# Optimization experiments

Measured on AMD Instinct MI355X. Metric: run time of the kernel, lower is better.

The kernel has to match this reference:

```python
import jax, jax.numpy as jnp
import numpy as np

IN_DIM = 128
KEY_F = 64
VAL_F = 128  # must equal IN_DIM for the residual
B, L = 8, 2048


def setup_inputs() -> dict:
    key = jax.random.key(0)
    ks = jax.random.split(key, 7)
    s_in = 1.0 / np.sqrt(IN_DIM)
    x = jax.random.normal(ks[0], (B, IN_DIM, L), dtype=jnp.float32)
    # Conv1d kernel_size=1 weights stored as [out, in]
    Wq = jax.random.uniform(ks[1], (KEY_F, IN_DIM), jnp.float32, -s_in, s_in)
    bq = jax.random.uniform(ks[2], (KEY_F,), jnp.float32, -s_in, s_in)
    Wk = jax.random.uniform(ks[3], (KEY_F, IN_DIM), jnp.float32, -s_in, s_in)
    bk = jax.random.uniform(ks[4], (KEY_F,), jnp.float32, -s_in, s_in)
    Wv = jax.random.uniform(ks[5], (VAL_F, IN_DIM), jnp.float32, -s_in, s_in)
    bv = jax.random.uniform(ks[6], (VAL_F,), jnp.float32, -s_in, s_in)
    gamma = jnp.zeros((1,), dtype=jnp.float32)
    return {"x": x, "Wq": Wq, "bq": bq, "Wk": Wk, "bk": bk, "Wv": Wv, "bv": bv, "gamma": gamma}


def reference(x, Wq, bq, Wk, bk, Wv, bv, gamma):
    # 1x1 conv projections: [B, C, L] -> [B, F, L]
    q = jnp.einsum('fc,bcl->bfl', Wq, x) + bq[None, :, None]
    k = jnp.einsum('fc,bcl->bfl', Wk, x) + bk[None, :, None]
    v = jnp.einsum('fc,bcl->bfl', Wv, x) + bv[None, :, None]
    # energy[b, i, j] = sum_f q[b, f, i] * k[b, f, j]  -> [B, L, L]
    energy = jnp.einsum('bfi,bfj->bij', q, k)
    attn = jax.nn.softmax(energy, axis=-1)
    # out[b, f, i] = sum_j attn[b, i, j] * v[b, f, j]
    out = jnp.einsum('bij,bfj->bfi', attn, v)
    return gamma * out + x
```

## Files before the change

### kernel.cpp

```cpp
#include <hip/hip_runtime.h>
#include <hip/hip_bf16.h>

#define LL 2048
#define NB 8
#define L2E 1.4426950408889634f

typedef float f32x4 __attribute__((ext_vector_type(4)));
typedef short s16x8 __attribute__((ext_vector_type(8)));
typedef unsigned int u32;

__device__ __forceinline__ unsigned short f2bf(float f) {
  u32 u = __float_as_uint(f);
  return (unsigned short)((u + 0x7FFFu + ((u >> 16) & 1u)) >> 16);
}

__global__ __launch_bounds__(256, 1) void proj_kernel(
    const float* __restrict__ x,
    const float* __restrict__ Wq, const float* __restrict__ bq,
    const float* __restrict__ Wk, const float* __restrict__ bk,
    const float* __restrict__ Wv, const float* __restrict__ bv,
    unsigned short* __restrict__ Qt,
    unsigned short* __restrict__ Kt,
    unsigned short* __restrict__ Vf)
{
  __shared__ float4 Wl[256 * 32];
  __shared__ float  bl[256];

  const int t = threadIdx.x;
  const float4* wq4 = (const float4*)Wq;
  const float4* wk4 = (const float4*)Wk;
  const float4* wv4 = (const float4*)Wv;
  #pragma unroll
  for (int i = 0; i < 8; ++i)  Wl[i * 256 + t]        = wq4[i * 256 + t];
  #pragma unroll
  for (int i = 0; i < 8; ++i)  Wl[2048 + i * 256 + t] = wk4[i * 256 + t];
  #pragma unroll
  for (int i = 0; i < 16; ++i) Wl[4096 + i * 256 + t] = wv4[i * 256 + t];
  bl[t] = (t < 64) ? bq[t] : (t < 128) ? bk[t - 64] : bv[t - 128];
  __syncthreads();

  const int fg = t >> 6;
  const int l  = t & 63;
  const int b  = blockIdx.y;
  const int gl = blockIdx.x * 64 + l;

  float acc[64];
  #pragma unroll
  for (int i = 0; i < 64; ++i) acc[i] = 0.f;

  const float* xb = x + (size_t)b * 128 * LL + gl;

  for (int c0 = 0; c0 < 128; c0 += 4) {
    float x0 = xb[(c0 + 0) * LL];
    float x1 = xb[(c0 + 1) * LL];
    float x2 = xb[(c0 + 2) * LL];
    float x3 = xb[(c0 + 3) * LL];
    #pragma unroll
    for (int ff = 0; ff < 64; ++ff) {
      float4 wv4v = Wl[(fg * 64 + ff) * 32 + (c0 >> 2)];
      acc[ff] = fmaf(x0, wv4v.x, acc[ff]);
      acc[ff] = fmaf(x1, wv4v.y, acc[ff]);
      acc[ff] = fmaf(x2, wv4v.z, acc[ff]);
      acc[ff] = fmaf(x3, wv4v.w, acc[ff]);
    }
  }
  #pragma unroll
  for (int ff = 0; ff < 64; ++ff) acc[ff] += bl[fg * 64 + ff];

  if (fg < 2) {
    unsigned short* dst = (fg == 0 ? Qt : Kt) + ((size_t)b * LL + gl) * 64;
    #pragma unroll
    for (int v = 0; v < 8; ++v) {
      s16x8 pk;
      #pragma unroll
      for (int e = 0; e < 8; ++e) pk[e] = (short)f2bf(acc[v * 8 + e]);
      *(s16x8*)(dst + v * 8) = pk;
    }
  } else {
    unsigned short* dst = Vf + ((size_t)b * 128 + (size_t)(fg - 2) * 64) * LL + gl;
    #pragma unroll
    for (int ff = 0; ff < 64; ++ff) dst[(size_t)ff * LL] = f2bf(acc[ff]);
  }
}

__global__ __launch_bounds__(256, 1) void attn_kernel(
    const unsigned short* __restrict__ Qt,
    const unsigned short* __restrict__ Kt,
    const unsigned short* __restrict__ Vf,
    const float* __restrict__ x,
    const float* __restrict__ gammap,
    float* __restrict__ out)
{
  __shared__ uint4 ldsK4[64 * 8];
  __shared__ uint4 ldsV4[128 * 8];
  __shared__ __align__(16) unsigned short Plds[4][16][80];
  __shared__ float Olds[4][16][129];

  const int t    = threadIdx.x;
  const int w    = t >> 6;
  const int lane = t & 63;
  const int cn   = lane & 15;
  const int g    = lane >> 4;
  const int bid  = blockIdx.x;
  const int virt = (bid & 7) * 32 + (bid >> 3);
  const int b    = virt >> 5;
  const int i0   = (virt & 31) * 64;

  s16x8 qf[2];
  {
    const unsigned short* qp = Qt + ((size_t)b * LL + i0 + w * 16 + cn) * 64 + g * 8;
    qf[0] = *(const s16x8*)(qp);
    qf[1] = *(const s16x8*)(qp + 32);
  }

  const f32x4 zero4 = {0.f, 0.f, 0.f, 0.f};
  f32x4 accO[8];
  #pragma unroll
  for (int i = 0; i < 8; ++i) accO[i] = zero4;
  float mrow[4], lrow[4];
  #pragma unroll
  for (int r = 0; r < 4; ++r) { mrow[r] = -1e30f; lrow[r] = 0.f; }

  for (int jt = 0; jt < 32; ++jt) {
    const int j0 = jt * 64;
    __syncthreads();

    #pragma unroll
    for (int e = 0; e < 2; ++e) {
      int q = e * 256 + t, r = q >> 3, c = q & 7;
      uint4 d = *(const uint4*)(Kt + ((size_t)b * LL + j0 + r) * 64 + c * 8);
      ldsK4[r * 8 + (c ^ (r & 7))] = d;
    }
    #pragma unroll
    for (int e = 0; e < 4; ++e) {
      int q = e * 256 + t, r = q >> 3, c = q & 7;
      uint4 d = *(const uint4*)(Vf + ((size_t)b * 128 + r) * LL + j0 + c * 8);
      ldsV4[r * 8 + (c ^ (r & 7))] = d;
    }
    __syncthreads();

    f32x4 s[4];
    #pragma unroll
    for (int jb = 0; jb < 4; ++jb) s[jb] = zero4;
    #pragma unroll
    for (int kt = 0; kt < 2; ++kt) {
      #pragma unroll
      for (int jb = 0; jb < 4; ++jb) {
        int r = jb * 16 + cn;
        s16x8 kf = *(const s16x8*)&ldsK4[r * 8 + ((kt * 4 + g) ^ (cn & 7))];
        s[jb] = __builtin_amdgcn_mfma_f32_16x16x32_bf16(qf[kt], kf, s[jb], 0, 0, 0);
      }
    }

    float tm[4];
    #pragma unroll
    for (int r = 0; r < 4; ++r) {
      tm[r] = fmaxf(fmaxf(s[0][r], s[1][r]), fmaxf(s[2][r], s[3][r]));
      tm[r] = fmaxf(tm[r], __shfl_xor(tm[r], 1));
      tm[r] = fmaxf(tm[r], __shfl_xor(tm[r], 2));
      tm[r] = fmaxf(tm[r], __shfl_xor(tm[r], 4));
      tm[r] = fmaxf(tm[r], __shfl_xor(tm[r], 8));
    }
    float alpha[4];
    #pragma unroll
    for (int r = 0; r < 4; ++r) {
      float mn = fmaxf(mrow[r], tm[r]);
      alpha[r] = __builtin_amdgcn_exp2f((mrow[r] - mn) * L2E);
      mrow[r] = mn;
    }
    float rs[4] = {0.f, 0.f, 0.f, 0.f};
    float p[4][4];
    #pragma unroll
    for (int jb = 0; jb < 4; ++jb) {
      #pragma unroll
      for (int r = 0; r < 4; ++r) {
        float pv = __builtin_amdgcn_exp2f((s[jb][r] - mrow[r]) * L2E);
        p[jb][r] = pv;
        rs[r] += pv;
      }
    }
    #pragma unroll
    for (int r = 0; r < 4; ++r) {
      rs[r] += __shfl_xor(rs[r], 1);
      rs[r] += __shfl_xor(rs[r], 2);
      rs[r] += __shfl_xor(rs[r], 4);
      rs[r] += __shfl_xor(rs[r], 8);
      lrow[r] = lrow[r] * alpha[r] + rs[r];
    }
    #pragma unroll
    for (int fb = 0; fb < 8; ++fb) {
      #pragma unroll
      for (int r = 0; r < 4; ++r) accO[fb][r] *= alpha[r];
    }

    #pragma unroll
    for (int jb = 0; jb < 4; ++jb) {
      #pragma unroll
      for (int r = 0; r < 4; ++r)
        Plds[w][g * 4 + r][jb * 16 + cn] = f2bf(p[jb][r]);
    }

    #pragma unroll
    for (int kt = 0; kt < 2; ++kt) {
      s16x8 pa = *(const s16x8*)((const unsigned short*)&Plds[w][cn][0] + kt * 32 + g * 8);
      #pragma unroll
      for (int fb = 0; fb < 8; ++fb) {
        int f = fb * 16 + cn;
        s16x8 vf = *(const s16x8*)&ldsV4[f * 8 + ((kt * 4 + g) ^ (cn & 7))];
        accO[fb] = __builtin_amdgcn_mfma_f32_16x16x32_bf16(pa, vf, accO[fb], 0, 0, 0);
      }
    }
  }

  #pragma unroll
  for (int r = 0; r < 4; ++r) {
    float inv = 1.f / lrow[r];
    #pragma unroll
    for (int fb = 0; fb < 8; ++fb)
      Olds[w][g * 4 + r][fb * 16 + cn] = accO[fb][r] * inv;
  }
  __syncthreads();
  const float gamma = gammap[0];
  {
    const int r = cn;
    const int row = i0 + w * 16 + r;
    #pragma unroll
    for (int ff = 0; ff < 32; ++ff) {
      int f = ff * 4 + g;
      float val = Olds[w][r][f];
      size_t idx = ((size_t)b * 128 + f) * LL + row;
      out[idx] = gamma * val + x[idx];
    }
  }
}

extern "C" void kernel_launch(void* const* d_in, const int* in_sizes, int n_in,
                              void* d_out, int out_size, void* d_ws, size_t ws_size,
                              hipStream_t stream) {
  const float* x     = (const float*)d_in[0];
  const float* Wq    = (const float*)d_in[1];
  const float* bq    = (const float*)d_in[2];
  const float* Wk    = (const float*)d_in[3];
  const float* bk    = (const float*)d_in[4];
  const float* Wv    = (const float*)d_in[5];
  const float* bv    = (const float*)d_in[6];
  const float* gamma = (const float*)d_in[7];
  float* out = (float*)d_out;

  unsigned short* Qt = (unsigned short*)d_ws;
  unsigned short* Kt = Qt + (size_t)NB * LL * 64;
  unsigned short* Vf = Kt + (size_t)NB * LL * 64;

  proj_kernel<<<dim3(32, 8), 256, 0, stream>>>(x, Wq, bq, Wk, bk, Wv, bv, Qt, Kt, Vf);
  attn_kernel<<<dim3(256), 256, 0, stream>>>(Qt, Kt, Vf, x, gamma, out);
}
```

Before: 197.2 us.

## Use MFMA for projections and double-buffer K/V tiles in attention

The projection kernel is rewritten to use bf16 MFMA instructions. Weights go into register fragments and x is staged transposed into LDS as bf16, replacing the scalar fp32 FMA loop. The attention kernel now double-buffers its K/V LDS tiles: each tile's global loads are issued into registers before the current tile's compute and written to the other buffer afterwards, which removes one barrier per iteration and hides load latency. In exchange it uses more LDS and registers, and the projections are now computed in bf16 rather than fp32, which lowers their precision.

```diff
diff --git a/kernel.cpp b/kernel.cpp
--- a/kernel.cpp
+++ b/kernel.cpp
@@ -8,10 +8,15 @@
 typedef float f32x4 __attribute__((ext_vector_type(4)));
 typedef short s16x8 __attribute__((ext_vector_type(8)));
 typedef unsigned int u32;
+typedef unsigned int u32x2 __attribute__((ext_vector_type(2)));
+typedef unsigned int u32x4 __attribute__((ext_vector_type(4)));
 
 __device__ __forceinline__ unsigned short f2bf(float f) {
   u32 u = __float_as_uint(f);
   return (unsigned short)((u + 0x7FFFu + ((u >> 16) & 1u)) >> 16);
+}
+__device__ __forceinline__ u32 pack2(float a, float b) {
+  return (u32)f2bf(a) | ((u32)f2bf(b) << 16);
 }
 
 __global__ __launch_bounds__(256, 1) void proj_kernel(
@@ -23,63 +28,108 @@
     unsigned short* __restrict__ Kt,
     unsigned short* __restrict__ Vf)
 {
-  __shared__ float4 Wl[256 * 32];
-  __shared__ float  bl[256];
-
-  const int t = threadIdx.x;
-  const float4* wq4 = (const float4*)Wq;
-  const float4* wk4 = (const float4*)Wk;
-  const float4* wv4 = (const float4*)Wv;
-  #pragma unroll
-  for (int i = 0; i < 8; ++i)  Wl[i * 256 + t]        = wq4[i * 256 + t];
-  #pragma unroll
-  for (int i = 0; i < 8; ++i)  Wl[2048 + i * 256 + t] = wk4[i * 256 + t];
-  #pragma unroll
-  for (int i = 0; i < 16; ++i) Wl[4096 + i * 256 + t] = wv4[i * 256 + t];
+  __shared__ __align__(16) unsigned short xT[64 * 128];
+  __shared__ float bl[256];
+
+  const int t  = threadIdx.x;
+  const int w  = t >> 6;
+  const int ll = t & 63;
+  const int lane = t & 63;
+  const int cn = lane & 15;
+  const int g  = lane >> 4;
+  const int b  = blockIdx.x >> 5;
+  const int l0 = (blockIdx.x & 31) * 64;
+
+  const int f0 = w * 64;
+  s16x8 afr[4][4];
+  #pragma unroll
+  for (int fb = 0; fb < 4; ++fb) {
+    const int f = f0 + fb * 16 + cn;
+    const float* p = (f < 64) ? (Wq + (size_t)f * 128)
+                   : (f < 128) ? (Wk + (size_t)(f - 64) * 128)
+                               : (Wv + (size_t)(f - 128) * 128);
+    #pragma unroll
+    for (int kt = 0; kt < 4; ++kt) {
+      const float4 u = *(const float4*)(p + kt * 32 + g * 8);
+      const float4 v = *(const float4*)(p + kt * 32 + g * 8 + 4);
+      u32x4 pk = {pack2(u.x, u.y), pack2(u.z, u.w), pack2(v.x, v.y), pack2(v.z, v.w)};
+      afr[fb][kt] = __builtin_bit_cast(s16x8, pk);
+    }
+  }
+
+  {
+    const float* xb = x + (size_t)b * 128 * LL + l0 + ll;
+    #pragma unroll
+    for (int it = 0; it < 4; ++it) {
+      const int ch = it * 4 + w;
+      const float* p = xb + (size_t)ch * 8 * LL;
+      float v[8];
+      #pragma unroll
+      for (int j = 0; j < 8; ++j) v[j] = p[(size_t)j * LL];
+      u32x4 pk = {pack2(v[0], v[1]), pack2(v[2], v[3]),
+                  pack2(v[4], v[5]), pack2(v[6], v[7])};
+      *(u32x4*)&xT[ll * 128 + ((ch ^ (ll & 15)) * 8)] = pk;
+    }
+  }
   bl[t] = (t < 64) ? bq[t] : (t < 128) ? bk[t - 64] : bv[t - 128];
   __syncthreads();
 
-  const int fg = t >> 6;
-  const int l  = t & 63;
-  const int b  = blockIdx.y;
-  const int gl = blockIdx.x * 64 + l;
-
-  float acc[64];
-  #pragma unroll
-  for (int i = 0; i < 64; ++i) acc[i] = 0.f;
-
-  const float* xb = x + (size_t)b * 128 * LL + gl;
-
-  for (int c0 = 0; c0 < 128; c0 += 4) {
-    float x0 = xb[(c0 + 0) * LL];
-    float x1 = xb[(c0 + 1) * LL];
-    float x2 = xb[(c0 + 2) * LL];
-    float x3 = xb[(c0 + 3) * LL];
-    #pragma unroll
-    for (int ff = 0; ff < 64; ++ff) {
-      float4 wv4v = Wl[(fg * 64 + ff) * 32 + (c0 >> 2)];
-      acc[ff] = fmaf(x0, wv4v.x, acc[ff]);
-      acc[ff] = fmaf(x1, wv4v.y, acc[ff]);
-      acc[ff] = fmaf(x2, wv4v.z, acc[ff]);
-      acc[ff] = fmaf(x3, wv4v.w, acc[ff]);
-    }
-  }
-  #pragma unroll
-  for (int ff = 0; ff < 64; ++ff) acc[ff] += bl[fg * 64 + ff];
-
-  if (fg < 2) {
-    unsigned short* dst = (fg == 0 ? Qt : Kt) + ((size_t)b * LL + gl) * 64;
-    #pragma unroll
-    for (int v = 0; v < 8; ++v) {
-      s16x8 pk;
-      #pragma unroll
-      for (int e = 0; e < 8; ++e) pk[e] = (short)f2bf(acc[v * 8 + e]);
-      *(s16x8*)(dst + v * 8) = pk;
+  const f32x4 zero4 = {0.f, 0.f, 0.f, 0.f};
+  f32x4 acc[4][4];
+  #pragma unroll
+  for (int fb = 0; fb < 4; ++fb)
+    #pragma unroll
+    for (int lb = 0; lb < 4; ++lb) acc[fb][lb] = zero4;
+
+  #pragma unroll
+  for (int kt = 0; kt < 4; ++kt) {
+    s16x8 bfr[4];
+    #pragma unroll
+    for (int lb = 0; lb < 4; ++lb)
+      bfr[lb] = *(const s16x8*)&xT[(lb * 16 + cn) * 128 + (((kt * 4 + g) ^ cn) * 8)];
+    #pragma unroll
+    for (int fb = 0; fb < 4; ++fb)
+      #pragma unroll
+      for (int lb = 0; lb < 4; ++lb)
+        acc[fb][lb] = __builtin_amdgcn_mfma_f32_16x16x32_bf16(afr[fb][kt], bfr[lb], acc[fb][lb], 0, 0, 0);
+  }
+
+  #pragma unroll
+  for (int fb = 0; fb < 4; ++fb) {
+    float bb0 = bl[f0 + fb * 16 + 4 * g + 0];
+    float bb1 = bl[f0 + fb * 16 + 4 * g + 1];
+    float bb2 = bl[f0 + fb * 16 + 4 * g + 2];
+    float bb3 = bl[f0 + fb * 16 + 4 * g + 3];
+    #pragma unroll
+    for (int lb = 0; lb < 4; ++lb) {
+      acc[fb][lb][0] += bb0; acc[fb][lb][1] += bb1;
+      acc[fb][lb][2] += bb2; acc[fb][lb][3] += bb3;
+    }
+  }
+
+  if (w < 2) {
+    unsigned short* base = (w == 0 ? Qt : Kt) + (size_t)b * LL * 64;
+    #pragma unroll
+    for (int lb = 0; lb < 4; ++lb) {
+      const int l = l0 + lb * 16 + cn;
+      #pragma unroll
+      for (int fb = 0; fb < 4; ++fb) {
+        u32x2 pk = {pack2(acc[fb][lb][0], acc[fb][lb][1]),
+                    pack2(acc[fb][lb][2], acc[fb][lb][3])};
+        *(u32x2*)(base + (size_t)l * 64 + fb * 16 + 4 * g) = pk;
+      }
     }
   } else {
-    unsigned short* dst = Vf + ((size_t)b * 128 + (size_t)(fg - 2) * 64) * LL + gl;
-    #pragma unroll
-    for (int ff = 0; ff < 64; ++ff) dst[(size_t)ff * LL] = f2bf(acc[ff]);
+    unsigned short* base = Vf + ((size_t)b * 128 + (size_t)(w - 2) * 64) * LL;
+    #pragma unroll
+    for (int fb = 0; fb < 4; ++fb)
+      #pragma unroll
+      for (int lb = 0; lb < 4; ++lb) {
+        const int l = l0 + lb * 16 + cn;
+        #pragma unroll
+        for (int r = 0; r < 4; ++r)
+          base[(size_t)(fb * 16 + 4 * g + r) * LL + l] = f2bf(acc[fb][lb][r]);
+      }
   }
 }
 
@@ -91,9 +141,9 @@
     const float* __restrict__ gammap,
     float* __restrict__ out)
 {
-  __shared__ uint4 ldsK4[64 * 8];
-  __shared__ uint4 ldsV4[128 * 8];
-  __shared__ __align__(16) unsigned short Plds[4][16][80];
+  __shared__ uint4 ldsK4[2][64 * 8];
+  __shared__ uint4 ldsV4[2][128 * 8];
+  __shared__ __align__(16) unsigned short Plds[4][16][72];
   __shared__ float Olds[4][16][129];
 
   const int t    = threadIdx.x;
@@ -113,6 +163,28 @@
     qf[1] = *(const s16x8*)(qp + 32);
   }
 
+  uint4 kreg[2], vreg[4];
+  const int sr_k[2] = { t >> 3, (256 + t) >> 3 };
+  const int sc     = t & 7;
+  const int sr_v[4] = { t >> 3, (256 + t) >> 3, (512 + t) >> 3, (768 + t) >> 3 };
+
+  auto issue_loads = [&](int j0) {
+    #pragma unroll
+    for (int e = 0; e < 2; ++e)
+      kreg[e] = *(const uint4*)(Kt + ((size_t)b * LL + j0 + sr_k[e]) * 64 + sc * 8);
+    #pragma unroll
+    for (int e = 0; e < 4; ++e)
+      vreg[e] = *(const uint4*)(Vf + ((size_t)b * 128 + sr_v[e]) * LL + j0 + sc * 8);
+  };
+  auto write_lds = [&](uint4* K4, uint4* V4) {
+    #pragma unroll
+    for (int e = 0; e < 2; ++e)
+      K4[sr_k[e] * 8 + (sc ^ (sr_k[e] & 7))] = kreg[e];
+    #pragma unroll
+    for (int e = 0; e < 4; ++e)
+      V4[sr_v[e] * 8 + (sc ^ (sr_v[e] & 7))] = vreg[e];
+  };
+
   const f32x4 zero4 = {0.f, 0.f, 0.f, 0.f};
   f32x4 accO[8];
   #pragma unroll
@@ -121,23 +193,17 @@
   #pragma unroll
   for (int r = 0; r < 4; ++r) { mrow[r] = -1e30f; lrow[r] = 0.f; }
 
+  issue_loads(0);
+  write_lds(ldsK4[0], ldsV4[0]);
+
   for (int jt = 0; jt < 32; ++jt) {
-    const int j0 = jt * 64;
+    const int cur = jt & 1;
     __syncthreads();
 
-    #pragma unroll
-    for (int e = 0; e < 2; ++e) {
-      int q = e * 256 + t, r = q >> 3, c = q & 7;
-      uint4 d = *(const uint4*)(Kt + ((size_t)b * LL + j0 + r) * 64 + c * 8);
-      ldsK4[r * 8 + (c ^ (r & 7))] = d;
-    }
-    #pragma unroll
-    for (int e = 0; e < 4; ++e) {
-      int q = e * 256 + t, r = q >> 3, c = q & 7;
-      uint4 d = *(const uint4*)(Vf + ((size_t)b * 128 + r) * LL + j0 + c * 8);
-      ldsV4[r * 8 + (c ^ (r & 7))] = d;
-    }
-    __syncthreads();
+    if (jt + 1 < 32) issue_loads((jt + 1) * 64);
+
+    const uint4* K4 = ldsK4[cur];
+    const uint4* V4 = ldsV4[cur];
 
     f32x4 s[4];
     #pragma unroll
@@ -147,7 +213,7 @@
       #pragma unroll
       for (int jb = 0; jb < 4; ++jb) {
         int r = jb * 16 + cn;
-        s16x8 kf = *(const s16x8*)&ldsK4[r * 8 + ((kt * 4 + g) ^ (cn & 7))];
+        s16x8 kf = *(const s16x8*)&K4[r * 8 + ((kt * 4 + g) ^ (r & 7))];
         s[jb] = __builtin_amdgcn_mfma_f32_16x16x32_bf16(qf[kt], kf, s[jb], 0, 0, 0);
       }
     }
@@ -206,10 +272,12 @@
       #pragma unroll
       for (int fb = 0; fb < 8; ++fb) {
         int f = fb * 16 + cn;
-        s16x8 vf = *(const s16x8*)&ldsV4[f * 8 + ((kt * 4 + g) ^ (cn & 7))];
+        s16x8 vf = *(const s16x8*)&V4[f * 8 + ((kt * 4 + g) ^ (f & 7))];
         accO[fb] = __builtin_amdgcn_mfma_f32_16x16x32_bf16(pa, vf, accO[fb], 0, 0, 0);
       }
     }
+
+    if (jt + 1 < 32) write_lds(ldsK4[cur ^ 1], ldsV4[cur ^ 1]);
   }
 
   #pragma unroll
@@ -251,6 +319,6 @@
   unsigned short* Kt = Qt + (size_t)NB * LL * 64;
   unsigned short* Vf = Kt + (size_t)NB * LL * 64;
 
-  proj_kernel<<<dim3(32, 8), 256, 0, stream>>>(x, Wq, bq, Wk, bk, Wv, bv, Qt, Kt, Vf);
+  proj_kernel<<<dim3(256), 256, 0, stream>>>(x, Wq, bq, Wk, bk, Wv, bv, Qt, Kt, Vf);
   attn_kernel<<<dim3(256), 256, 0, stream>>>(Qt, Kt, Vf, x, gamma, out);
 }
```

Result: faster. 167.9 us (-14.8%).
